# Performance work log

Measured on AMD Instinct MI355X. Metric: run time of the kernel, lower is better.

Reference implementation:

```python
import jax, jax.numpy as jnp
import numpy as np

HEADS = 8
HEAD_DIM = 64
FOLD = 2   # fold_w == fold_h
PROP = 2   # proposal_w == proposal_h -> M = PROP*PROP centers
DIM = 512


def _conv1x1(x, w, b):
    # x: [B,C,H,W], w: [O,C] (1x1 conv kernel squeezed), b: [O]
    return jnp.einsum('bchw,oc->bohw', x, w) + b[None, :, None, None]


def _normalize(x):
    # F.normalize along last dim (eps-clamped L2 norm)
    n = jnp.linalg.norm(x, axis=-1, keepdims=True)
    return x / jnp.maximum(n, 1e-12)


def _fold(t, f):
    # 'b c (f1 w) (f2 h) -> (b f1 f2) c w h'
    b, c, W, H = t.shape
    return t.reshape(b, c, f, W // f, f, H // f).transpose(0, 2, 4, 1, 3, 5).reshape(b * f * f, c, W // f, H // f)


def _unfold(t, f):
    # '(b f1 f2) c w h -> b c (f1 w) (f2 h)'
    bf, c, w, h = t.shape
    b = bf // (f * f)
    return t.reshape(b, f, f, c, w, h).transpose(0, 3, 1, 4, 2, 5).reshape(b, c, f * w, f * h)


def _pool(t, p):
    # AdaptiveAvgPool2d((p,p)) when spatial dims divisible by p
    b, c, W, H = t.shape
    return t.reshape(b, c, p, W // p, p, H // p).mean(axis=(3, 5))


def reference(x, f_w, f_b, v_w, v_b, proj_w, proj_b, sim_alpha, sim_beta):
    B = x.shape[0]
    value = _conv1x1(x, v_w, v_b)
    feat = _conv1x1(x, f_w, f_b)
    # split heads: 'b (e c) w h -> (b e) c w h'
    feat = feat.reshape(B * HEADS, HEAD_DIM, feat.shape[2], feat.shape[3])
    value = value.reshape(B * HEADS, HEAD_DIM, value.shape[2], value.shape[3])
    feat = _fold(feat, FOLD)
    value = _fold(value, FOLD)
    b, c, w, h = feat.shape

    centers = _pool(feat, PROP)                                   # [b,c,p,p]
    value_centers = _pool(value, PROP).reshape(b, c, -1).transpose(0, 2, 1)  # [b,M,c]
    cflat = centers.reshape(b, c, -1).transpose(0, 2, 1)          # [b,M,c]
    M = cflat.shape[1]
    xflat = feat.reshape(b, c, -1).transpose(0, 2, 1)             # [b,N,c]

    cos = jnp.einsum('bmc,bnc->bmn', _normalize(cflat), _normalize(xflat))
    sim = jax.nn.sigmoid(sim_beta + sim_alpha * cos)              # [b,M,N]

    idx = jnp.argmax(sim, axis=1)                                 # [b,N] hard assignment
    sim_max = jnp.max(sim, axis=1)
    L_Clst = -jnp.mean(sim_max)
    mask = jax.nn.one_hot(idx, M, dtype=sim.dtype).transpose(0, 2, 1)  # [b,M,N]
    L_Sep = jnp.mean(jnp.max(sim * (1.0 - mask), axis=1))
    Cn = _normalize(cflat)
    G = jnp.einsum('bmc,bkc->bmk', Cn, Cn)
    L_Orth = jnp.mean((G - jnp.eye(M, dtype=G.dtype)) ** 2)

    sim_m = sim * mask
    vflat = value.reshape(b, c, -1).transpose(0, 2, 1)            # [b,N,c]
    # scatter_sum of values into their assigned cluster == one-hot matmul
    agg = jnp.einsum('bmn,bnc->bmc', mask, vflat)                 # [b,M,c]
    counts = mask.sum(axis=-1, keepdims=True)                     # [b,M,1]
    out = (agg + value_centers) / (counts + 1.0)                  # [b,M,c]
    # masked weighted broadcast back to points (avoids [b,M,N,c] intermediate)
    outp = jnp.einsum('bmn,bmc->bnc', sim_m, out)                 # [b,N,c]
    outp = outp.transpose(0, 2, 1).reshape(b, c, w, h)
    outp = _unfold(outp, FOLD)
    outp = outp.reshape(B, HEADS * HEAD_DIM, outp.shape[2], outp.shape[3])
    outp = _conv1x1(outp, proj_w, proj_b)
    return outp, jnp.stack([L_Orth, L_Clst, L_Sep])


def setup_inputs():
    key = jax.random.key(0)
    ks = jax.random.split(key, 4)
    E = HEADS * HEAD_DIM  # 512
    return {
        'x': jax.random.normal(ks[0], (32, DIM, 32, 32), jnp.float32),
        'f_w': jax.random.normal(ks[1], (E, DIM), jnp.float32) * 0.02,
        'f_b': jnp.zeros((E,), jnp.float32),
        'v_w': jax.random.normal(ks[2], (E, DIM), jnp.float32) * 0.02,
        'v_b': jnp.zeros((E,), jnp.float32),
        'proj_w': jax.random.normal(ks[3], (DIM, E), jnp.float32) * 0.02,
        'proj_b': jnp.zeros((DIM,), jnp.float32),
        'sim_alpha': jnp.ones((1,), jnp.float32),
        'sim_beta': jnp.zeros((1,), jnp.float32),
    }
```

## Files before the change

kernel.cpp:

```cpp
#include <hip/hip_runtime.h>


#define HW 1024

typedef _Float16 f16x8 __attribute__((ext_vector_type(8)));
typedef float f32x4 __attribute__((ext_vector_type(4)));

union H4 { uint2 u; _Float16 h[4]; };
union H8 { uint4 u; _Float16 h[8]; };
union H2 { unsigned int u; _Float16 h[2]; };
union F4 { float4 v; float f[4]; };

__device__ __forceinline__ void gld16(const _Float16* g, _Float16* l) {
    __builtin_amdgcn_global_load_lds(
        (const __attribute__((address_space(1))) void*)g,
        (__attribute__((address_space(3))) void*)l, 16, 0, 0);
}

__global__ __launch_bounds__(256) void k_wsplit(
    const float* __restrict__ fw, const float* __restrict__ vw,
    _Float16* __restrict__ fwh, _Float16* __restrict__ fwl,
    _Float16* __restrict__ vwh)
{
    const int i = (blockIdx.x * 256 + threadIdx.x) * 4;
    F4 a;
    a.v = *(const float4*)&fw[i];
    H4 h, l;
#pragma unroll
    for (int j = 0; j < 4; ++j) {
        const float s = a.f[j] * 256.f;
        h.h[j] = (_Float16)s;
        l.h[j] = (_Float16)(s - (float)h.h[j]);
    }
    *(uint2*)&fwh[i] = h.u;
    *(uint2*)&fwl[i] = l.u;
    a.v = *(const float4*)&vw[i];
#pragma unroll
    for (int j = 0; j < 4; ++j) h.h[j] = (_Float16)(a.f[j] * 256.f);
    *(uint2*)&vwh[i] = h.u;
}

__global__ __launch_bounds__(256) void k_xsplit(
    const float* __restrict__ x,
    _Float16* __restrict__ xh, _Float16* __restrict__ xl)
{
    __shared__ float tile[64][65];
    const int t = threadIdx.x;
    const int b = blockIdx.z;
    const int k0 = blockIdx.y * 64;
    const int n0 = blockIdx.x * 64;
    const float* Xb = x + (size_t)b * (512 * HW);

#pragma unroll
    for (int j = 0; j < 16; ++j) {
        const int k = j * 4 + (t >> 6);
        const int n = t & 63;
        tile[k][n] = Xb[(size_t)(k0 + k) * HW + n0 + n];
    }
    __syncthreads();
#pragma unroll
    for (int j = 0; j < 8; ++j) {
        const int n = j * 8 + (t >> 5);
        const int kp = t & 31;
        const float s0 = tile[kp * 2][n] * 256.f;
        const float s1 = tile[kp * 2 + 1][n] * 256.f;
        H2 hh, hl;
        hh.h[0] = (_Float16)s0;
        hh.h[1] = (_Float16)s1;
        hl.h[0] = (_Float16)(s0 - (float)hh.h[0]);
        hl.h[1] = (_Float16)(s1 - (float)hh.h[1]);
        const size_t o = ((size_t)b * 1024 + n0 + n) * 512 + k0 + kp * 2;
        *(unsigned int*)&xh[o] = hh.u;
        *(unsigned int*)&xl[o] = hl.u;
    }
}

__global__ __launch_bounds__(512, 2) void k_feat(
    const _Float16* __restrict__ fwh, const _Float16* __restrict__ fwl,
    const float* __restrict__ bias,
    const _Float16* __restrict__ xh, const _Float16* __restrict__ xl,
    float* __restrict__ feat_T, float* __restrict__ centers_f)
{
    __shared__ _Float16 Ah[2][8192], Al[2][8192], Bh[2][8192], Bl[2][8192];
    __shared__ float pool_lds[4][4][256];
    const int t = threadIdx.x, lane = t & 63, wv = t >> 6;
    const int b = blockIdx.z, o0 = blockIdx.y * 256, p0 = blockIdx.x * 256;
    const int wr = wv >> 2, wc = wv & 3;

    f32x4 acc[8][4];
#pragma unroll
    for (int i = 0; i < 8; ++i)
#pragma unroll
        for (int j = 0; j < 4; ++j) acc[i][j] = (f32x4){0.f, 0.f, 0.f, 0.f};

    const int gslot = ((lane & 3) ^ ((lane >> 3) & 3)) * 8;
    const _Float16* ash = fwh + (size_t)(o0 + wv * 32 + (lane >> 2)) * 512 + gslot;
    const _Float16* asl = fwl + (size_t)(o0 + wv * 32 + (lane >> 2)) * 512 + gslot;
    const size_t brow = (size_t)b * 1024 + p0 + wv * 32 + (lane >> 2);
    const _Float16* bsh = xh + brow * 512 + gslot;
    const _Float16* bsl = xl + brow * 512 + gslot;

#define STAGE_F(d, k0)                                              \
    {                                                               \
        gld16(ash + (k0),        &Ah[(d)][(wv * 32) * 32]);         \
        gld16(ash + (k0) + 8192, &Ah[(d)][(wv * 32 + 16) * 32]);    \
        gld16(asl + (k0),        &Al[(d)][(wv * 32) * 32]);         \
        gld16(asl + (k0) + 8192, &Al[(d)][(wv * 32 + 16) * 32]);    \
        gld16(bsh + (k0),        &Bh[(d)][(wv * 32) * 32]);         \
        gld16(bsh + (k0) + 8192, &Bh[(d)][(wv * 32 + 16) * 32]);    \
        gld16(bsl + (k0),        &Bl[(d)][(wv * 32) * 32]);         \
        gld16(bsl + (k0) + 8192, &Bl[(d)][(wv * 32 + 16) * 32]);    \
    }

    STAGE_F(0, 0);
    const int slA = ((lane >> 4) ^ ((lane >> 1) & 3)) * 8;
    int cur = 0;
    for (int kb = 0; kb < 16; ++kb) {
        if (kb < 15) {
            STAGE_F(cur ^ 1, (kb + 1) * 32);
            asm volatile("s_waitcnt vmcnt(8)" ::: "memory");
        } else {
            asm volatile("s_waitcnt vmcnt(0)" ::: "memory");
        }
        __builtin_amdgcn_sched_barrier(0);
        __builtin_amdgcn_s_barrier();
        f16x8 bh4[4], bl4[4];
#pragma unroll
        for (int j = 0; j < 4; ++j) {
            const int bo = (wc * 64 + j * 16 + (lane & 15)) * 32 + slA;
            bh4[j] = *(f16x8*)&Bh[cur][bo];
            bl4[j] = *(f16x8*)&Bl[cur][bo];
        }
#pragma unroll
        for (int mi = 0; mi < 8; ++mi) {
            const int ao = (wr * 128 + mi * 16 + (lane & 15)) * 32 + slA;
            const f16x8 ah = *(f16x8*)&Ah[cur][ao];
            const f16x8 al = *(f16x8*)&Al[cur][ao];
#pragma unroll
            for (int nj = 0; nj < 4; ++nj) {
                acc[mi][nj] = __builtin_amdgcn_mfma_f32_16x16x32_f16(ah, bh4[nj], acc[mi][nj], 0, 0, 0);
                acc[mi][nj] = __builtin_amdgcn_mfma_f32_16x16x32_f16(ah, bl4[nj], acc[mi][nj], 0, 0, 0);
                acc[mi][nj] = __builtin_amdgcn_mfma_f32_16x16x32_f16(al, bh4[nj], acc[mi][nj], 0, 0, 0);
            }
        }
        __builtin_amdgcn_s_barrier();
        cur ^= 1;
    }
#undef STAGE_F

    const int pj = (lane >> 3) & 1;
    float ps[32][2];
#pragma unroll
    for (int mi = 0; mi < 8; ++mi) {
        const int obase = o0 + wr * 128 + mi * 16 + (lane >> 4) * 4;
        F4 bs4;
        bs4.v = *(const float4*)&bias[obase];
#pragma unroll
        for (int r = 0; r < 4; ++r) { ps[mi * 4 + r][0] = 0.f; ps[mi * 4 + r][1] = 0.f; }
#pragma unroll
        for (int nj = 0; nj < 4; ++nj) {
            const int p = p0 + wc * 64 + nj * 16 + (lane & 15);
            F4 vv;
#pragma unroll
            for (int r = 0; r < 4; ++r) {
                vv.f[r] = acc[mi][nj][r] * (1.f / 65536.f) + bs4.f[r];
                ps[mi * 4 + r][nj & 1] += vv.f[r];
            }
            *(float4*)&feat_T[((size_t)b * 1024 + p) * 512 + obase] = vv.v;
        }
    }
#pragma unroll
    for (int q = 0; q < 32; ++q)
#pragma unroll
        for (int f2s = 0; f2s < 2; ++f2s) {
            ps[q][f2s] += __shfl_xor(ps[q][f2s], 1);
            ps[q][f2s] += __shfl_xor(ps[q][f2s], 2);
            ps[q][f2s] += __shfl_xor(ps[q][f2s], 4);
        }
    if ((lane & 7) == 0) {
#pragma unroll
        for (int mi = 0; mi < 8; ++mi)
#pragma unroll
            for (int r = 0; r < 4; ++r) {
                const int ol = wr * 128 + mi * 16 + (lane >> 4) * 4 + r;
                pool_lds[wc][0 * 2 + pj][ol] = ps[mi * 4 + r][0];
                pool_lds[wc][1 * 2 + pj][ol] = ps[mi * 4 + r][1];
            }
    }
    __syncthreads();
#pragma unroll
    for (int u = 0; u < 2; ++u) {
        const int idx = u * 512 + t;
        const int g = idx >> 8, o = idx & 255;
        const float s = pool_lds[0][g][o] + pool_lds[1][g][o]
                      + pool_lds[2][g][o] + pool_lds[3][g][o];
        centers_f[(((size_t)b * 8 + 2 * blockIdx.x) * 4 + g) * 512 + o0 + o] = s;
        centers_f[(((size_t)b * 8 + 2 * blockIdx.x + 1) * 4 + g) * 512 + o0 + o] = 0.f;
    }
}

__global__ __launch_bounds__(256) void k_value(
    const _Float16* __restrict__ vwh, const float* __restrict__ bias,
    const _Float16* __restrict__ xh,
    _Float16* __restrict__ value_T, float* __restrict__ centers_v)
{
    __shared__ _Float16 Ah[2][4096], Bh[2][4096];
    __shared__ float pool_lds[2][128][4];
    const int t = threadIdx.x, lane = t & 63, wv = t >> 6;
    const int b = blockIdx.z, o0 = blockIdx.y * 128, p0 = blockIdx.x * 128;
    const int wr = wv >> 1, wc = wv & 1;

    f32x4 acc[4][4];
#pragma unroll
    for (int i = 0; i < 4; ++i)
#pragma unroll
        for (int j = 0; j < 4; ++j) acc[i][j] = (f32x4){0.f, 0.f, 0.f, 0.f};

    const int gslot = ((lane & 3) ^ ((lane >> 3) & 3)) * 8;
    const _Float16* ash = vwh + (size_t)(o0 + wv * 32 + (lane >> 2)) * 512 + gslot;
    const _Float16* bsh = xh + ((size_t)b * 1024 + p0 + wv * 32 + (lane >> 2)) * 512 + gslot;

#define STAGE_V(d, k0)                                              \
    {                                                               \
        gld16(ash + (k0),        &Ah[(d)][(wv * 32) * 32]);         \
        gld16(ash + (k0) + 8192, &Ah[(d)][(wv * 32 + 16) * 32]);    \
        gld16(bsh + (k0),        &Bh[(d)][(wv * 32) * 32]);         \
        gld16(bsh + (k0) + 8192, &Bh[(d)][(wv * 32 + 16) * 32]);    \
    }

    STAGE_V(0, 0);
    const int slA = ((lane >> 4) ^ ((lane >> 1) & 3)) * 8;
    int cur = 0;
    for (int kb = 0; kb < 16; ++kb) {
        if (kb < 15) {
            STAGE_V(cur ^ 1, (kb + 1) * 32);
            asm volatile("s_waitcnt vmcnt(4)" ::: "memory");
        } else {
            asm volatile("s_waitcnt vmcnt(0)" ::: "memory");
        }
        __builtin_amdgcn_sched_barrier(0);
        __builtin_amdgcn_s_barrier();
        f16x8 ah4[4], bh4[4];
#pragma unroll
        for (int i = 0; i < 4; ++i) {
            ah4[i] = *(f16x8*)&Ah[cur][(wr * 64 + i * 16 + (lane & 15)) * 32 + slA];
            bh4[i] = *(f16x8*)&Bh[cur][(wc * 64 + i * 16 + (lane & 15)) * 32 + slA];
        }
#pragma unroll
        for (int mi = 0; mi < 4; ++mi)
#pragma unroll
            for (int nj = 0; nj < 4; ++nj)
                acc[mi][nj] = __builtin_amdgcn_mfma_f32_16x16x32_f16(ah4[mi], bh4[nj], acc[mi][nj], 0, 0, 0);
        __builtin_amdgcn_s_barrier();
        cur ^= 1;
    }
#undef STAGE_V

    const int pj = (lane >> 3) & 1;
    float ps[16][2];
#pragma unroll
    for (int mi = 0; mi < 4; ++mi) {
        const int obase = o0 + wr * 64 + mi * 16 + (lane >> 4) * 4;
        F4 bs4;
        bs4.v = *(const float4*)&bias[obase];
#pragma unroll
        for (int r = 0; r < 4; ++r) { ps[mi * 4 + r][0] = 0.f; ps[mi * 4 + r][1] = 0.f; }
#pragma unroll
        for (int nj = 0; nj < 4; ++nj) {
            const int p = p0 + wc * 64 + nj * 16 + (lane & 15);
            H4 hv;
#pragma unroll
            for (int r = 0; r < 4; ++r) {
                const float v = acc[mi][nj][r] * (1.f / 65536.f) + bs4.f[r];
                ps[mi * 4 + r][nj & 1] += v;
                hv.h[r] = (_Float16)v;
            }
            *(uint2*)&value_T[((size_t)b * 1024 + p) * 512 + obase] = hv.u;
        }
    }
#pragma unroll
    for (int q = 0; q < 16; ++q)
#pragma unroll
        for (int f2s = 0; f2s < 2; ++f2s) {
            ps[q][f2s] += __shfl_xor(ps[q][f2s], 1);
            ps[q][f2s] += __shfl_xor(ps[q][f2s], 2);
            ps[q][f2s] += __shfl_xor(ps[q][f2s], 4);
        }
    if ((lane & 7) == 0) {
#pragma unroll
        for (int mi = 0; mi < 4; ++mi)
#pragma unroll
            for (int r = 0; r < 4; ++r) {
                const int ol = wr * 64 + mi * 16 + (lane >> 4) * 4 + r;
                pool_lds[wc][ol][0 * 2 + pj] = ps[mi * 4 + r][0];
                pool_lds[wc][ol][1 * 2 + pj] = ps[mi * 4 + r][1];
            }
    }
    __syncthreads();
#pragma unroll
    for (int u = 0; u < 2; ++u) {
        const int idx = u * 256 + t;
        const int g = idx >> 7, o = idx & 127;
        centers_v[(((size_t)b * 8 + blockIdx.x) * 4 + g) * 512 + o0 + o] =
            pool_lds[0][o][g] + pool_lds[1][o][g];
    }
}

__global__ __launch_bounds__(256) void k_cluster(
    const float* __restrict__ feat_T, const _Float16* __restrict__ value_T,
    const float* __restrict__ centers_f, const float* __restrict__ centers_v,
    const float* __restrict__ alpha_p, const float* __restrict__ beta_p,
    _Float16* __restrict__ outpT, float* __restrict__ part)
{
    __shared__ _Float16 vbuf[256 * 64];
    __shared__ float cnl[4][64];
    __shared__ float vcl[4][64];
    __shared__ float obuf[4][68];
    __shared__ int   sidx[256];
    __shared__ float sbest[256];
    __shared__ float scrt[4][4][64];
    __shared__ int   cntw[4][4];
    __shared__ float red[8];
    __shared__ float gsc[16];

    const int t = threadIdx.x, lane = t & 63, wv = t >> 6;
    const int bp = blockIdx.x;
    const int f2 = bp & 1, f1 = (bp >> 1) & 1, head = (bp >> 2) & 7, b = bp >> 5;

    const int m = wv, cc = lane;
    const int pi = m >> 1, pj = m & 1, g = f2 * 2 + pj;
    const int pt = 4 * f1 + 2 * pi;
    {
        const float* cf = centers_f + (((size_t)b * 8 + pt) * 4 + g) * 512 + head * 64 + cc;
        const float c = (cf[0] + cf[4 * 512]) * (1.f / 64.f);
        float ss = c * c;
#pragma unroll
        for (int off = 32; off > 0; off >>= 1) ss += __shfl_xor(ss, off);
        const float inv = 1.f / fmaxf(sqrtf(ss), 1e-12f);
        cnl[m][cc] = c * inv;
        const float* cv = centers_v + (((size_t)b * 8 + pt) * 4 + g) * 512 + head * 64 + cc;
        vcl[m][cc] = (cv[0] + cv[4 * 512]) * (1.f / 64.f);
    }
    __syncthreads();

    if (t < 16) {
        const int gm = t >> 2, gk = t & 3;
        float gg = 0.f;
        for (int c = 0; c < 64; ++c) gg += cnl[gm][c] * cnl[gk][c];
        const float d = gg - (gm == gk ? 1.f : 0.f);
        gsc[t] = d * d;
    }

    const float alpha = alpha_p[0], beta = beta_p[0];
    const int n = t;
    const int pg = (f1 * 16 + (n >> 4)) * 32 + f2 * 16 + (n & 15);
    const float* fp = feat_T + ((size_t)b * 1024 + pg) * 512 + head * 64;
    float ssf = 0.f, d0 = 0.f, d1 = 0.f, d2 = 0.f, d3 = 0.f;
#pragma unroll
    for (int c4 = 0; c4 < 16; ++c4) {
        F4 fv;
        fv.v = *(const float4*)&fp[c4 * 4];
        const float4 c0 = *(const float4*)&cnl[0][c4 * 4];
        const float4 c1 = *(const float4*)&cnl[1][c4 * 4];
        const float4 c2 = *(const float4*)&cnl[2][c4 * 4];
        const float4 c3 = *(const float4*)&cnl[3][c4 * 4];
        ssf += fv.f[0]*fv.f[0] + fv.f[1]*fv.f[1] + fv.f[2]*fv.f[2] + fv.f[3]*fv.f[3];
        d0 += fv.f[0]*c0.x + fv.f[1]*c0.y + fv.f[2]*c0.z + fv.f[3]*c0.w;
        d1 += fv.f[0]*c1.x + fv.f[1]*c1.y + fv.f[2]*c1.z + fv.f[3]*c1.w;
        d2 += fv.f[0]*c2.x + fv.f[1]*c2.y + fv.f[2]*c2.z + fv.f[3]*c2.w;
        d3 += fv.f[0]*c3.x + fv.f[1]*c3.y + fv.f[2]*c3.z + fv.f[3]*c3.w;
    }
    const float invf = 1.f / fmaxf(sqrtf(ssf), 1e-12f);
    float simv[4];
    simv[0] = d0 * invf;
    simv[1] = d1 * invf;
    simv[2] = d2 * invf;
    simv[3] = d3 * invf;
#pragma unroll
    for (int mm = 0; mm < 4; ++mm)
        simv[mm] = 1.f / (1.f + expf(-(beta + alpha * simv[mm])));
    float best = simv[0], second = -1.f;
    int idx = 0;
#pragma unroll
    for (int mm = 1; mm < 4; ++mm) {
        if (simv[mm] > best) { second = best; best = simv[mm]; idx = mm; }
        else second = fmaxf(second, simv[mm]);
    }
    sidx[n] = idx;
    sbest[n] = best;

    const _Float16* vp = value_T + ((size_t)b * 1024 + pg) * 512 + head * 64;
#pragma unroll
    for (int j = 0; j < 8; ++j) {
        const uint4 v = *(const uint4*)&vp[j * 8];
        *(uint4*)&vbuf[n * 64 + ((j * 8) ^ ((n & 7) << 3))] = v;
    }

    float bsum = best, s2sum = second;
#pragma unroll
    for (int off = 32; off > 0; off >>= 1) {
        bsum += __shfl_xor(bsum, off);
        s2sum += __shfl_xor(s2sum, off);
    }
    if (lane == 0) { red[wv] = bsum; red[4 + wv] = s2sum; }
    __syncthreads();
    if (t == 0) {
        part[bp]        = gsc[0] + gsc[1] + gsc[2] + gsc[3] + gsc[4] + gsc[5] + gsc[6] + gsc[7]
                        + gsc[8] + gsc[9] + gsc[10] + gsc[11] + gsc[12] + gsc[13] + gsc[14] + gsc[15];
        part[1024 + bp] = red[0] + red[1] + red[2] + red[3];
        part[2048 + bp] = red[4] + red[5] + red[6] + red[7];
    }

    {
        float ag0 = 0.f, ag1 = 0.f, ag2 = 0.f, ag3 = 0.f;
        int c0i = 0, c1i = 0, c2i = 0, c3i = 0;
        for (int j = 0; j < 64; ++j) {
            const int nn = wv * 64 + j;
            const int id = sidx[nn];
            const float v = (float)vbuf[nn * 64 + (cc ^ ((nn & 7) << 3))];
            ag0 += (id == 0) ? v : 0.f;  c0i += (id == 0);
            ag1 += (id == 1) ? v : 0.f;  c1i += (id == 1);
            ag2 += (id == 2) ? v : 0.f;  c2i += (id == 2);
            ag3 += (id == 3) ? v : 0.f;  c3i += (id == 3);
        }
        scrt[wv][0][cc] = ag0;
        scrt[wv][1][cc] = ag1;
        scrt[wv][2][cc] = ag2;
        scrt[wv][3][cc] = ag3;
        if (lane == 0) {
            cntw[wv][0] = c0i; cntw[wv][1] = c1i;
            cntw[wv][2] = c2i; cntw[wv][3] = c3i;
        }
    }
    __syncthreads();

    {
        const float a = scrt[0][m][cc] + scrt[1][m][cc] + scrt[2][m][cc] + scrt[3][m][cc];
        const int c = cntw[0][m] + cntw[1][m] + cntw[2][m] + cntw[3][m];
        obuf[m][cc] = (a + vcl[m][cc]) / (float)(c + 1);
    }
    __syncthreads();

    const int cch = (t & 3) * 16;
#pragma unroll
    for (int r = 0; r < 4; ++r) {
        const int nn = r * 64 + (t >> 2);
        const int id = sidx[nn];
        const float bs = sbest[nn];
        const int p = (f1 * 16 + (nn >> 4)) * 32 + f2 * 16 + (nn & 15);
        _Float16* dst = outpT + (((size_t)b * 8 + head) * 1024 + p) * 64 + cch;
        const float4 oa = *(const float4*)&obuf[id][cch];
        const float4 ob = *(const float4*)&obuf[id][cch + 4];
        const float4 oc = *(const float4*)&obuf[id][cch + 8];
        const float4 od = *(const float4*)&obuf[id][cch + 12];
        H8 w0, w1;
        w0.h[0] = (_Float16)(bs * oa.x); w0.h[1] = (_Float16)(bs * oa.y);
        w0.h[2] = (_Float16)(bs * oa.z); w0.h[3] = (_Float16)(bs * oa.w);
        w0.h[4] = (_Float16)(bs * ob.x); w0.h[5] = (_Float16)(bs * ob.y);
        w0.h[6] = (_Float16)(bs * ob.z); w0.h[7] = (_Float16)(bs * ob.w);
        w1.h[0] = (_Float16)(bs * oc.x); w1.h[1] = (_Float16)(bs * oc.y);
        w1.h[2] = (_Float16)(bs * oc.z); w1.h[3] = (_Float16)(bs * oc.w);
        w1.h[4] = (_Float16)(bs * od.x); w1.h[5] = (_Float16)(bs * od.y);
        w1.h[6] = (_Float16)(bs * od.z); w1.h[7] = (_Float16)(bs * od.w);
        *(uint4*)dst = w0.u;
        *(uint4*)(dst + 8) = w1.u;
    }
}

__global__ __launch_bounds__(256) void k_proj(
    const float* __restrict__ w, const float* __restrict__ bias,
    const _Float16* __restrict__ outpT,
    const float* __restrict__ part,
    float* __restrict__ dout)
{
    __shared__ _Float16 As[2][4096], Bs[2][4096];
    __shared__ float fin[12];
    const int t = threadIdx.x, lane = t & 63, wv = t >> 6;

    if (blockIdx.x == 0 && blockIdx.y == 0 && blockIdx.z == 0) {
        float so = part[t] + part[t + 256] + part[t + 512] + part[t + 768];
        float sc = part[1024 + t] + part[1280 + t] + part[1536 + t] + part[1792 + t];
        float sp = part[2048 + t] + part[2304 + t] + part[2560 + t] + part[2816 + t];
#pragma unroll
        for (int off = 32; off > 0; off >>= 1) {
            so += __shfl_xor(so, off);
            sc += __shfl_xor(sc, off);
            sp += __shfl_xor(sp, off);
        }
        if (lane == 0) { fin[wv] = so; fin[4 + wv] = sc; fin[8 + wv] = sp; }
        __syncthreads();
        if (t == 0) {
            dout[16777216]     = (fin[0] + fin[1] + fin[2] + fin[3]) / 16384.f;
            dout[16777216 + 1] = -(fin[4] + fin[5] + fin[6] + fin[7]) / 262144.f;
            dout[16777216 + 2] = (fin[8] + fin[9] + fin[10] + fin[11]) / 262144.f;
        }
        __syncthreads();
    }

    const int b = blockIdx.z, o0 = blockIdx.y * 128, p0 = blockIdx.x * 128;
    const int wr = wv >> 1, wc = wv & 1;

    f32x4 acc[4][4];
#pragma unroll
    for (int i = 0; i < 4; ++i)
#pragma unroll
        for (int j = 0; j < 4; ++j) acc[i][j] = (f32x4){0.f, 0.f, 0.f, 0.f};

    const int gslot = ((lane & 3) ^ ((lane >> 3) & 3)) * 8;
    const int srow = p0 + wv * 32 + (lane >> 2);
    const int arow_l = t >> 3;
    const int aq = t & 7;
    const int aqs = aq ^ (((t >> 4) & 3) << 1);

    F4 av[4];
#define LOADA(k0)                                                        \
    {                                                                    \
        _Pragma("unroll")                                                \
        for (int j = 0; j < 4; ++j)                                      \
            av[j].v = *(const float4*)&w[(size_t)(o0 + j * 32 + arow_l) * 512 + (k0) + aq * 4]; \
    }
#define WRITEA(d)                                                        \
    {                                                                    \
        _Pragma("unroll")                                                \
        for (int j = 0; j < 4; ++j) {                                    \
            H4 hh;                                                       \
            _Pragma("unroll")                                            \
            for (int i = 0; i < 4; ++i) hh.h[i] = (_Float16)(av[j].f[i] * 256.f); \
            *(uint2*)&As[(d)][(j * 32 + arow_l) * 32 + aqs * 4] = hh.u;  \
        }                                                                \
    }
#define STAGEB(d, kb)                                                    \
    {                                                                    \
        const _Float16* bsrc = outpT + (((size_t)b * 8 + ((kb) >> 1)) * 1024 + srow) * 64 \
                               + ((kb) & 1) * 32 + gslot;                \
        gld16(bsrc,        &Bs[(d)][(wv * 32) * 32]);                    \
        gld16(bsrc + 1024, &Bs[(d)][(wv * 32 + 16) * 32]);               \
    }

    LOADA(0);
    STAGEB(0, 0);
    WRITEA(0);
    __syncthreads();
    const int slA = ((lane >> 4) ^ ((lane >> 1) & 3)) * 8;
    int cur = 0;
    for (int kb = 0; kb < 16; ++kb) {
        if (kb < 15) {
            LOADA((kb + 1) * 32);
            STAGEB(cur ^ 1, kb + 1);
        }
        f16x8 ah4[4], bh4[4];
#pragma unroll
        for (int i = 0; i < 4; ++i) {
            ah4[i] = *(f16x8*)&As[cur][(wr * 64 + i * 16 + (lane & 15)) * 32 + slA];
            bh4[i] = *(f16x8*)&Bs[cur][(wc * 64 + i * 16 + (lane & 15)) * 32 + slA];
        }
#pragma unroll
        for (int mi = 0; mi < 4; ++mi)
#pragma unroll
            for (int nj = 0; nj < 4; ++nj)
                acc[mi][nj] = __builtin_amdgcn_mfma_f32_16x16x32_f16(ah4[mi], bh4[nj], acc[mi][nj], 0, 0, 0);
        if (kb < 15) WRITEA(cur ^ 1);
        __syncthreads();
        cur ^= 1;
    }
#undef LOADA
#undef WRITEA
#undef STAGEB

#pragma unroll
    for (int mi = 0; mi < 4; ++mi)
#pragma unroll
        for (int r = 0; r < 4; ++r) {
            const int o = o0 + wr * 64 + mi * 16 + (lane >> 4) * 4 + r;
            const float bs = bias[o];
#pragma unroll
            for (int nj = 0; nj < 4; ++nj) {
                const int p = p0 + wc * 64 + nj * 16 + (lane & 15);
                dout[((size_t)b * 512 + o) * HW + p] = acc[mi][nj][r] * (1.f / 256.f) + bs;
            }
        }
}

extern "C" void kernel_launch(void* const* d_in, const int* in_sizes, int n_in,
                              void* d_out, int out_size, void* d_ws, size_t ws_size,
                              hipStream_t stream)
{
    const float* x   = (const float*)d_in[0];
    const float* f_w = (const float*)d_in[1];
    const float* f_b = (const float*)d_in[2];
    const float* v_w = (const float*)d_in[3];
    const float* v_b = (const float*)d_in[4];
    const float* p_w = (const float*)d_in[5];
    const float* p_b = (const float*)d_in[6];
    const float* s_a = (const float*)d_in[7];
    const float* s_b = (const float*)d_in[8];
    float* out = (float*)d_out;

    char* ws = (char*)d_ws;
    float*     feat_T  = (float*)ws;
    _Float16*  xh      = (_Float16*)(ws + (size_t)64 * 1024 * 1024);
    _Float16*  xl      = (_Float16*)(ws + (size_t)96 * 1024 * 1024);
    _Float16*  outpT   = xh;
    _Float16*  value_T = xl;
    float*     part    = (float*)(ws + (size_t)128 * 1024 * 1024);

    _Float16* fwh       = (_Float16*)out;
    _Float16* fwl       = (_Float16*)(out + 131072);
    _Float16* vwh       = (_Float16*)(out + 262144);
    float*    centers_f = out + 393216;
    float*    centers_v = out + 917504;

    k_wsplit <<<dim3(256), 256, 0, stream>>>(f_w, v_w, fwh, fwl, vwh);
    k_xsplit <<<dim3(16, 8, 32), 256, 0, stream>>>(x, xh, xl);
    k_feat   <<<dim3(4, 2, 32), 512, 0, stream>>>(fwh, fwl, f_b, xh, xl, feat_T, centers_f);
    k_value  <<<dim3(8, 4, 32), 256, 0, stream>>>(vwh, v_b, xh, value_T, centers_v);
    k_cluster<<<dim3(1024), 256, 0, stream>>>(feat_T, value_T, centers_f, centers_v,
                                              s_a, s_b, outpT, part);
    k_proj   <<<dim3(8, 4, 32), 256, 0, stream>>>(p_w, p_b, outpT, part, out);
}
```

Baseline: 191.9 us.

## Fuse value projection GEMM into feature GEMM kernel and drop value LDS staging

The separate value 1x1-conv GEMM kernel is merged into the feature GEMM kernel, so each block runs a second K loop over the same x tile with the value weights, reusing its LDS buffers and 256x256 tiling. This removes one kernel launch and lets the value GEMM use larger tiles. The cluster kernel no longer stages value rows in LDS and instead reads value_T straight from global memory in a strided per-channel pattern. The layout of the output scratch offsets also moves. Risks are a longer serialized kernel with fewer blocks, and uncoalesced strided global reads in the cluster kernel.

```diff
diff --git a/kernel.cpp b/kernel.cpp
--- a/kernel.cpp
+++ b/kernel.cpp
@@ -75,11 +75,13 @@
     }
 }
 
-__global__ __launch_bounds__(512, 2) void k_feat(
+__global__ __launch_bounds__(512, 2) void k_featval(
     const _Float16* __restrict__ fwh, const _Float16* __restrict__ fwl,
-    const float* __restrict__ bias,
+    const _Float16* __restrict__ vwh,
+    const float* __restrict__ f_b, const float* __restrict__ v_b,
     const _Float16* __restrict__ xh, const _Float16* __restrict__ xl,
-    float* __restrict__ feat_T, float* __restrict__ centers_f)
+    float* __restrict__ feat_T, float* __restrict__ centers_f,
+    _Float16* __restrict__ value_T, float* __restrict__ centers_v)
 {
     __shared__ _Float16 Ah[2][8192], Al[2][8192], Bh[2][8192], Bl[2][8192];
     __shared__ float pool_lds[4][4][256];
@@ -96,6 +98,7 @@
     const int gslot = ((lane & 3) ^ ((lane >> 3) & 3)) * 8;
     const _Float16* ash = fwh + (size_t)(o0 + wv * 32 + (lane >> 2)) * 512 + gslot;
     const _Float16* asl = fwl + (size_t)(o0 + wv * 32 + (lane >> 2)) * 512 + gslot;
+    const _Float16* asv = vwh + (size_t)(o0 + wv * 32 + (lane >> 2)) * 512 + gslot;
     const size_t brow = (size_t)b * 1024 + p0 + wv * 32 + (lane >> 2);
     const _Float16* bsh = xh + brow * 512 + gslot;
     const _Float16* bsl = xl + brow * 512 + gslot;
@@ -111,6 +114,13 @@
         gld16(bsl + (k0),        &Bl[(d)][(wv * 32) * 32]);         \
         gld16(bsl + (k0) + 8192, &Bl[(d)][(wv * 32 + 16) * 32]);    \
     }
+#define STAGE_W(d, k0)                                              \
+    {                                                               \
+        gld16(asv + (k0),        &Ah[(d)][(wv * 32) * 32]);         \
+        gld16(asv + (k0) + 8192, &Ah[(d)][(wv * 32 + 16) * 32]);    \
+        gld16(bsh + (k0),        &Bh[(d)][(wv * 32) * 32]);         \
+        gld16(bsh + (k0) + 8192, &Bh[(d)][(wv * 32 + 16) * 32]);    \
+    }
 
     STAGE_F(0, 0);
     const int slA = ((lane >> 4) ^ ((lane >> 1) & 3)) * 8;
@@ -146,163 +156,145 @@
         __builtin_amdgcn_s_barrier();
         cur ^= 1;
     }
-#undef STAGE_F
+
+    STAGE_W(0, 0);
 
     const int pj = (lane >> 3) & 1;
-    float ps[32][2];
-#pragma unroll
-    for (int mi = 0; mi < 8; ++mi) {
-        const int obase = o0 + wr * 128 + mi * 16 + (lane >> 4) * 4;
-        F4 bs4;
-        bs4.v = *(const float4*)&bias[obase];
-#pragma unroll
-        for (int r = 0; r < 4; ++r) { ps[mi * 4 + r][0] = 0.f; ps[mi * 4 + r][1] = 0.f; }
-#pragma unroll
-        for (int nj = 0; nj < 4; ++nj) {
-            const int p = p0 + wc * 64 + nj * 16 + (lane & 15);
-            F4 vv;
-#pragma unroll
-            for (int r = 0; r < 4; ++r) {
-                vv.f[r] = acc[mi][nj][r] * (1.f / 65536.f) + bs4.f[r];
-                ps[mi * 4 + r][nj & 1] += vv.f[r];
+    {
+        float ps[32][2];
+#pragma unroll
+        for (int mi = 0; mi < 8; ++mi) {
+            const int obase = o0 + wr * 128 + mi * 16 + (lane >> 4) * 4;
+            F4 bs4;
+            bs4.v = *(const float4*)&f_b[obase];
+#pragma unroll
+            for (int r = 0; r < 4; ++r) { ps[mi * 4 + r][0] = 0.f; ps[mi * 4 + r][1] = 0.f; }
+#pragma unroll
+            for (int nj = 0; nj < 4; ++nj) {
+                const int p = p0 + wc * 64 + nj * 16 + (lane & 15);
+                F4 vv;
+#pragma unroll
+                for (int r = 0; r < 4; ++r) {
+                    vv.f[r] = acc[mi][nj][r] * (1.f / 65536.f) + bs4.f[r];
+                    ps[mi * 4 + r][nj & 1] += vv.f[r];
+                }
+                *(float4*)&feat_T[((size_t)b * 1024 + p) * 512 + obase] = vv.v;
             }
-            *(float4*)&feat_T[((size_t)b * 1024 + p) * 512 + obase] = vv.v;
-        }
-    }
-#pragma unroll
-    for (int q = 0; q < 32; ++q)
-#pragma unroll
-        for (int f2s = 0; f2s < 2; ++f2s) {
-            ps[q][f2s] += __shfl_xor(ps[q][f2s], 1);
-            ps[q][f2s] += __shfl_xor(ps[q][f2s], 2);
-            ps[q][f2s] += __shfl_xor(ps[q][f2s], 4);
-        }
-    if ((lane & 7) == 0) {
-#pragma unroll
-        for (int mi = 0; mi < 8; ++mi)
-#pragma unroll
-            for (int r = 0; r < 4; ++r) {
-                const int ol = wr * 128 + mi * 16 + (lane >> 4) * 4 + r;
-                pool_lds[wc][0 * 2 + pj][ol] = ps[mi * 4 + r][0];
-                pool_lds[wc][1 * 2 + pj][ol] = ps[mi * 4 + r][1];
+        }
+#pragma unroll
+        for (int q = 0; q < 32; ++q)
+#pragma unroll
+            for (int f2s = 0; f2s < 2; ++f2s) {
+                ps[q][f2s] += __shfl_xor(ps[q][f2s], 1);
+                ps[q][f2s] += __shfl_xor(ps[q][f2s], 2);
+                ps[q][f2s] += __shfl_xor(ps[q][f2s], 4);
             }
-    }
-    __syncthreads();
-#pragma unroll
-    for (int u = 0; u < 2; ++u) {
-        const int idx = u * 512 + t;
-        const int g = idx >> 8, o = idx & 255;
-        const float s = pool_lds[0][g][o] + pool_lds[1][g][o]
-                      + pool_lds[2][g][o] + pool_lds[3][g][o];
-        centers_f[(((size_t)b * 8 + 2 * blockIdx.x) * 4 + g) * 512 + o0 + o] = s;
-        centers_f[(((size_t)b * 8 + 2 * blockIdx.x + 1) * 4 + g) * 512 + o0 + o] = 0.f;
-    }
-}
-
-__global__ __launch_bounds__(256) void k_value(
-    const _Float16* __restrict__ vwh, const float* __restrict__ bias,
-    const _Float16* __restrict__ xh,
-    _Float16* __restrict__ value_T, float* __restrict__ centers_v)
-{
-    __shared__ _Float16 Ah[2][4096], Bh[2][4096];
-    __shared__ float pool_lds[2][128][4];
-    const int t = threadIdx.x, lane = t & 63, wv = t >> 6;
-    const int b = blockIdx.z, o0 = blockIdx.y * 128, p0 = blockIdx.x * 128;
-    const int wr = wv >> 1, wc = wv & 1;
-
-    f32x4 acc[4][4];
-#pragma unroll
-    for (int i = 0; i < 4; ++i)
-#pragma unroll
-        for (int j = 0; j < 4; ++j) acc[i][j] = (f32x4){0.f, 0.f, 0.f, 0.f};
-
-    const int gslot = ((lane & 3) ^ ((lane >> 3) & 3)) * 8;
-    const _Float16* ash = vwh + (size_t)(o0 + wv * 32 + (lane >> 2)) * 512 + gslot;
-    const _Float16* bsh = xh + ((size_t)b * 1024 + p0 + wv * 32 + (lane >> 2)) * 512 + gslot;
-
-#define STAGE_V(d, k0)                                              \
-    {                                                               \
-        gld16(ash + (k0),        &Ah[(d)][(wv * 32) * 32]);         \
-        gld16(ash + (k0) + 8192, &Ah[(d)][(wv * 32 + 16) * 32]);    \
-        gld16(bsh + (k0),        &Bh[(d)][(wv * 32) * 32]);         \
-        gld16(bsh + (k0) + 8192, &Bh[(d)][(wv * 32 + 16) * 32]);    \
-    }
-
-    STAGE_V(0, 0);
-    const int slA = ((lane >> 4) ^ ((lane >> 1) & 3)) * 8;
-    int cur = 0;
+        if ((lane & 7) == 0) {
+#pragma unroll
+            for (int mi = 0; mi < 8; ++mi)
+#pragma unroll
+                for (int r = 0; r < 4; ++r) {
+                    const int ol = wr * 128 + mi * 16 + (lane >> 4) * 4 + r;
+                    pool_lds[wc][0 * 2 + pj][ol] = ps[mi * 4 + r][0];
+                    pool_lds[wc][1 * 2 + pj][ol] = ps[mi * 4 + r][1];
+                }
+        }
+        __syncthreads();
+#pragma unroll
+        for (int u = 0; u < 2; ++u) {
+            const int idx = u * 512 + t;
+            const int g = idx >> 8, o = idx & 255;
+            const float s = pool_lds[0][g][o] + pool_lds[1][g][o]
+                          + pool_lds[2][g][o] + pool_lds[3][g][o];
+            centers_f[(((size_t)b * 8 + 2 * blockIdx.x) * 4 + g) * 512 + o0 + o] = s;
+            centers_f[(((size_t)b * 8 + 2 * blockIdx.x + 1) * 4 + g) * 512 + o0 + o] = 0.f;
+        }
+    }
+
+    f32x4 vacc[8][4];
+#pragma unroll
+    for (int i = 0; i < 8; ++i)
+#pragma unroll
+        for (int j = 0; j < 4; ++j) vacc[i][j] = (f32x4){0.f, 0.f, 0.f, 0.f};
+
+    cur = 0;
     for (int kb = 0; kb < 16; ++kb) {
         if (kb < 15) {
-            STAGE_V(cur ^ 1, (kb + 1) * 32);
+            STAGE_W(cur ^ 1, (kb + 1) * 32);
             asm volatile("s_waitcnt vmcnt(4)" ::: "memory");
         } else {
             asm volatile("s_waitcnt vmcnt(0)" ::: "memory");
         }
         __builtin_amdgcn_sched_barrier(0);
         __builtin_amdgcn_s_barrier();
-        f16x8 ah4[4], bh4[4];
-#pragma unroll
-        for (int i = 0; i < 4; ++i) {
-            ah4[i] = *(f16x8*)&Ah[cur][(wr * 64 + i * 16 + (lane & 15)) * 32 + slA];
-            bh4[i] = *(f16x8*)&Bh[cur][(wc * 64 + i * 16 + (lane & 15)) * 32 + slA];
-        }
-#pragma unroll
-        for (int mi = 0; mi < 4; ++mi)
+        f16x8 bh4[4];
+#pragma unroll
+        for (int j = 0; j < 4; ++j)
+            bh4[j] = *(f16x8*)&Bh[cur][(wc * 64 + j * 16 + (lane & 15)) * 32 + slA];
+#pragma unroll
+        for (int mi = 0; mi < 8; ++mi) {
+            const f16x8 ah = *(f16x8*)&Ah[cur][(wr * 128 + mi * 16 + (lane & 15)) * 32 + slA];
 #pragma unroll
             for (int nj = 0; nj < 4; ++nj)
-                acc[mi][nj] = __builtin_amdgcn_mfma_f32_16x16x32_f16(ah4[mi], bh4[nj], acc[mi][nj], 0, 0, 0);
+                vacc[mi][nj] = __builtin_amdgcn_mfma_f32_16x16x32_f16(ah, bh4[nj], vacc[mi][nj], 0, 0, 0);
+        }
         __builtin_amdgcn_s_barrier();
         cur ^= 1;
     }
-#undef STAGE_V
-
-    const int pj = (lane >> 3) & 1;
-    float ps[16][2];
-#pragma unroll
-    for (int mi = 0; mi < 4; ++mi) {
-        const int obase = o0 + wr * 64 + mi * 16 + (lane >> 4) * 4;
-        F4 bs4;
-        bs4.v = *(const float4*)&bias[obase];
-#pragma unroll
-        for (int r = 0; r < 4; ++r) { ps[mi * 4 + r][0] = 0.f; ps[mi * 4 + r][1] = 0.f; }
-#pragma unroll
-        for (int nj = 0; nj < 4; ++nj) {
-            const int p = p0 + wc * 64 + nj * 16 + (lane & 15);
-            H4 hv;
-#pragma unroll
-            for (int r = 0; r < 4; ++r) {
-                const float v = acc[mi][nj][r] * (1.f / 65536.f) + bs4.f[r];
-                ps[mi * 4 + r][nj & 1] += v;
-                hv.h[r] = (_Float16)v;
+#undef STAGE_F
+#undef STAGE_W
+
+    {
+        float ps[32][2];
+#pragma unroll
+        for (int mi = 0; mi < 8; ++mi) {
+            const int obase = o0 + wr * 128 + mi * 16 + (lane >> 4) * 4;
+            F4 bs4;
+            bs4.v = *(const float4*)&v_b[obase];
+#pragma unroll
+            for (int r = 0; r < 4; ++r) { ps[mi * 4 + r][0] = 0.f; ps[mi * 4 + r][1] = 0.f; }
+#pragma unroll
+            for (int nj = 0; nj < 4; ++nj) {
+                const int p = p0 + wc * 64 + nj * 16 + (lane & 15);
+                H4 hv;
+#pragma unroll
+                for (int r = 0; r < 4; ++r) {
+                    const float v = vacc[mi][nj][r] * (1.f / 65536.f) + bs4.f[r];
+                    ps[mi * 4 + r][nj & 1] += v;
+                    hv.h[r] = (_Float16)v;
+                }
+                *(uint2*)&value_T[((size_t)b * 1024 + p) * 512 + obase] = hv.u;
             }
-            *(uint2*)&value_T[((size_t)b * 1024 + p) * 512 + obase] = hv.u;
-        }
-    }
-#pragma unroll
-    for (int q = 0; q < 16; ++q)
-#pragma unroll
-        for (int f2s = 0; f2s < 2; ++f2s) {
-            ps[q][f2s] += __shfl_xor(ps[q][f2s], 1);
-            ps[q][f2s] += __shfl_xor(ps[q][f2s], 2);
-            ps[q][f2s] += __shfl_xor(ps[q][f2s], 4);
-        }
-    if ((lane & 7) == 0) {
-#pragma unroll
-        for (int mi = 0; mi < 4; ++mi)
-#pragma unroll
-            for (int r = 0; r < 4; ++r) {
-                const int ol = wr * 64 + mi * 16 + (lane >> 4) * 4 + r;
-                pool_lds[wc][ol][0 * 2 + pj] = ps[mi * 4 + r][0];
-                pool_lds[wc][ol][1 * 2 + pj] = ps[mi * 4 + r][1];
+        }
+#pragma unroll
+        for (int q = 0; q < 32; ++q)
+#pragma unroll
+            for (int f2s = 0; f2s < 2; ++f2s) {
+                ps[q][f2s] += __shfl_xor(ps[q][f2s], 1);
+                ps[q][f2s] += __shfl_xor(ps[q][f2s], 2);
+                ps[q][f2s] += __shfl_xor(ps[q][f2s], 4);
             }
-    }
-    __syncthreads();
-#pragma unroll
-    for (int u = 0; u < 2; ++u) {
-        const int idx = u * 256 + t;
-        const int g = idx >> 7, o = idx & 127;
-        centers_v[(((size_t)b * 8 + blockIdx.x) * 4 + g) * 512 + o0 + o] =
-            pool_lds[0][o][g] + pool_lds[1][o][g];
+        __syncthreads();
+        if ((lane & 7) == 0) {
+#pragma unroll
+            for (int mi = 0; mi < 8; ++mi)
+#pragma unroll
+                for (int r = 0; r < 4; ++r) {
+                    const int ol = wr * 128 + mi * 16 + (lane >> 4) * 4 + r;
+                    pool_lds[wc][0 * 2 + pj][ol] = ps[mi * 4 + r][0];
+                    pool_lds[wc][1 * 2 + pj][ol] = ps[mi * 4 + r][1];
+                }
+        }
+        __syncthreads();
+#pragma unroll
+        for (int u = 0; u < 2; ++u) {
+            const int idx = u * 512 + t;
+            const int g = idx >> 8, o = idx & 255;
+            const float s = pool_lds[0][g][o] + pool_lds[1][g][o]
+                          + pool_lds[2][g][o] + pool_lds[3][g][o];
+            centers_v[(((size_t)b * 8 + 2 * blockIdx.x) * 4 + g) * 512 + o0 + o] = s;
+            centers_v[(((size_t)b * 8 + 2 * blockIdx.x + 1) * 4 + g) * 512 + o0 + o] = 0.f;
+        }
     }
 }
 
@@ -312,7 +304,6 @@
     const float* __restrict__ alpha_p, const float* __restrict__ beta_p,
     _Float16* __restrict__ outpT, float* __restrict__ part)
 {
-    __shared__ _Float16 vbuf[256 * 64];
     __shared__ float cnl[4][64];
     __shared__ float vcl[4][64];
     __shared__ float obuf[4][68];
@@ -389,13 +380,6 @@
     sidx[n] = idx;
     sbest[n] = best;
 
-    const _Float16* vp = value_T + ((size_t)b * 1024 + pg) * 512 + head * 64;
-#pragma unroll
-    for (int j = 0; j < 8; ++j) {
-        const uint4 v = *(const uint4*)&vp[j * 8];
-        *(uint4*)&vbuf[n * 64 + ((j * 8) ^ ((n & 7) << 3))] = v;
-    }
-
     float bsum = best, s2sum = second;
 #pragma unroll
     for (int off = 32; off > 0; off >>= 1) {
@@ -412,12 +396,16 @@
     }
 
     {
+        const _Float16* vT = value_T + ((size_t)b * 1024) * 512 + head * 64 + cc;
+        const int rowbase = (f1 * 16 + wv * 4) * 32 + f2 * 16;
         float ag0 = 0.f, ag1 = 0.f, ag2 = 0.f, ag3 = 0.f;
         int c0i = 0, c1i = 0, c2i = 0, c3i = 0;
+#pragma unroll 8
         for (int j = 0; j < 64; ++j) {
             const int nn = wv * 64 + j;
             const int id = sidx[nn];
-            const float v = (float)vbuf[nn * 64 + (cc ^ ((nn & 7) << 3))];
+            const int pgn = rowbase + (j >> 4) * 32 + (j & 15);
+            const float v = (float)vT[(size_t)pgn * 512];
             ag0 += (id == 0) ? v : 0.f;  c0i += (id == 0);
             ag1 += (id == 1) ? v : 0.f;  c1i += (id == 1);
             ag2 += (id == 2) ? v : 0.f;  c2i += (id == 2);
@@ -607,13 +595,13 @@
     _Float16* fwh       = (_Float16*)out;
     _Float16* fwl       = (_Float16*)(out + 131072);
     _Float16* vwh       = (_Float16*)(out + 262144);
-    float*    centers_f = out + 393216;
-    float*    centers_v = out + 917504;
+    float*    centers_f = out + 524288;
+    float*    centers_v = out + 1048576;
 
     k_wsplit <<<dim3(256), 256, 0, stream>>>(f_w, v_w, fwh, fwl, vwh);
     k_xsplit <<<dim3(16, 8, 32), 256, 0, stream>>>(x, xh, xl);
-    k_feat   <<<dim3(4, 2, 32), 512, 0, stream>>>(fwh, fwl, f_b, xh, xl, feat_T, centers_f);
-    k_value  <<<dim3(8, 4, 32), 256, 0, stream>>>(vwh, v_b, xh, value_T, centers_v);
+    k_featval<<<dim3(4, 2, 32), 512, 0, stream>>>(fwh, fwl, vwh, f_b, v_b, xh, xl,
+                                                  feat_T, centers_f, value_T, centers_v);
     k_cluster<<<dim3(1024), 256, 0, stream>>>(feat_T, value_T, centers_f, centers_v,
                                               s_a, s_b, outpT, part);
     k_proj   <<<dim3(8, 4, 32), 256, 0, stream>>>(p_w, p_b, outpT, part, out);
```

Measured after the change: 186.0 us. 1.03x faster.
